# Kernel optimization log

Measured on AMD Instinct MI355X. Metric: run time of the kernel, lower is better.

## Reference

```python
import jax, jax.numpy as jnp
import numpy as np

D_MODEL = 1024
H = 16
D_K = D_MODEL // H
B = 128   # batch (intersample attention attends across this dim)
N = 256   # samples / tokens per row


def setup_inputs() -> dict:
    key = jax.random.key(0)
    ks = jax.random.split(key, 8)
    s = 1.0 / np.sqrt(D_MODEL)
    return {
        "query": jax.random.normal(ks[0], (B, N, D_MODEL), jnp.float32),
        "key":   jax.random.normal(ks[1], (B, N, D_MODEL), jnp.float32),
        "value": jax.random.normal(ks[2], (B, N, D_MODEL), jnp.float32),
        "Wq": jax.random.normal(ks[3], (D_MODEL, D_MODEL), jnp.float32) * s,
        "bq": jnp.zeros((D_MODEL,), jnp.float32),
        "Wk": jax.random.normal(ks[4], (D_MODEL, D_MODEL), jnp.float32) * s,
        "bk": jnp.zeros((D_MODEL,), jnp.float32),
        "Wv": jax.random.normal(ks[5], (D_MODEL, D_MODEL), jnp.float32) * s,
        "bv": jnp.zeros((D_MODEL,), jnp.float32),
        "Wo": jax.random.normal(ks[6], (D_MODEL, D_MODEL), jnp.float32) * s,
        "bo": jnp.zeros((D_MODEL,), jnp.float32),
    }


def _proj_heads(x, W, b):
    # torch nn.Linear: x @ W.T + b ; then view (b, n, h, d_k) -> (b, h, n, d_k)
    y = jnp.einsum('bnd,ed->bne', x, W) + b
    bsz, n, _ = y.shape
    return y.reshape(bsz, n, H, D_K).transpose(0, 2, 1, 3)


def reference(query, key, value, Wq, bq, Wk, bk, Wv, bv, Wo, bo):
    q = _proj_heads(query, Wq, bq)  # (b, h, n, d_k)
    k = _proj_heads(key,   Wk, bk)
    v = _proj_heads(value, Wv, bv)
    # intersample attention: attend ACROSS the batch dim b (per head, per sample n)
    scale = 1.0 / jnp.sqrt(jnp.asarray(D_K, q.dtype))
    scores = jnp.einsum('bhnd,chnd->hnbc', q, k) * scale  # (h, n, b, b)
    p = jax.nn.softmax(scores, axis=-1)
    out = jnp.einsum('hnbc,chnd->bhnd', p, v)             # (b, h, n, d_k)
    # merge heads: (b, h, n, d_k) -> (b, n, h*d_k)
    bsz, _, n, _ = out.shape
    out = out.transpose(0, 2, 1, 3).reshape(bsz, n, H * D_K)
    return jnp.einsum('bnd,ed->bne', out, Wo) + bo
```

## Files before the change

kernel.cpp:

```cpp
#include <hip/hip_runtime.h>
#include <hip/hip_bf16.h>
#include <stdint.h>

#define D_MODEL 1024
#define HEADS   16
#define DK      64
#define BATCH   128
#define NTOK    256
#define MROWS   (BATCH * NTOK)

typedef __attribute__((ext_vector_type(8))) short bf16x8;
typedef __attribute__((ext_vector_type(4))) float f32x4;

__device__ __forceinline__ unsigned short f2b_rne(float f) {
    union { float f; unsigned int u; } c; c.f = f;
    unsigned int u = c.u;
    unsigned int r = (u + 0x7FFFu + ((u >> 16) & 1u)) >> 16;
    return (unsigned short)r;
}

__device__ __forceinline__ void async16(const void* g, void* l) {
    __builtin_amdgcn_global_load_lds(
        (__attribute__((address_space(1))) void*)g,
        (__attribute__((address_space(3))) void*)l,
        16, 0, 0);
}

__global__ __launch_bounds__(256)
void f2b_kernel(const float* __restrict__ x, ushort* __restrict__ y, int n4) {
    int i = blockIdx.x * blockDim.x + threadIdx.x;
    int stride = gridDim.x * blockDim.x;
    for (; i < n4; i += stride) {
        float4 v = ((const float4*)x)[i];
        ushort4 o;
        o.x = f2b_rne(v.x); o.y = f2b_rne(v.y);
        o.z = f2b_rne(v.z); o.w = f2b_rne(v.w);
        ((ushort4*)y)[i] = o;
    }
}

template<int MODE>
__global__ __launch_bounds__(256)
void gemm_nt(const ushort* __restrict__ A, const ushort* __restrict__ B,
             const float* __restrict__ bias, void* __restrict__ Cout,
             int M, int N, int K, float alpha)
{
    __shared__ ushort As[128 * 32];
    __shared__ ushort Bs[128 * 32];

    const int tid  = threadIdx.x;
    const int wave = tid >> 6, lane = tid & 63;
    const int quad = lane >> 4, l15 = lane & 15;
    const int pm = blockIdx.x * 128, pn = blockIdx.y * 128;
    const int wm = (wave & 1) * 64, wn = (wave >> 1) * 64;

    f32x4 acc[4][4] = {};

    const int rg = lane >> 2;
    const int c8 = (lane & 3) * 8;
    const ushort* Abase0 = A + (size_t)(pm + wave * 32 + rg) * K + c8;
    const ushort* Abase1 = Abase0 + (size_t)16 * K;
    const ushort* Bbase0 = B + (size_t)(pn + wave * 32 + rg) * K + c8;
    const ushort* Bbase1 = Bbase0 + (size_t)16 * K;

    for (int k0 = 0; k0 < K; k0 += 32) {
        __syncthreads();
        async16(Abase0 + k0, &As[wave * 1024]);
        async16(Abase1 + k0, &As[wave * 1024 + 512]);
        async16(Bbase0 + k0, &Bs[wave * 1024]);
        async16(Bbase1 + k0, &Bs[wave * 1024 + 512]);
        __syncthreads();

        bf16x8 af[4], bfr[4];
        #pragma unroll
        for (int t = 0; t < 4; t++) {
            af[t]  = *(const bf16x8*)&As[(wm + t * 16 + l15) * 32 + quad * 8];
            bfr[t] = *(const bf16x8*)&Bs[(wn + t * 16 + l15) * 32 + quad * 8];
        }
        #pragma unroll
        for (int i = 0; i < 4; i++)
            #pragma unroll
            for (int j = 0; j < 4; j++)
                acc[i][j] = __builtin_amdgcn_mfma_f32_16x16x32_bf16(af[i], bfr[j], acc[i][j], 0, 0, 0);
    }

    if (MODE == 0) {
        ushort* out = (ushort*)Cout;
        #pragma unroll
        for (int i = 0; i < 4; i++) {
            const int mbase = pm + wm + i * 16 + quad * 4;
            #pragma unroll
            for (int j = 0; j < 4; j++) {
                const int e = pn + wn + j * 16 + l15;
                const float bv = bias[e];
                const int h = e >> 6, d = e & 63;
                #pragma unroll
                for (int r = 0; r < 4; r++) {
                    const int mm = mbase + r;
                    const int bb = mm >> 8, nn = mm & 255;
                    float val = (acc[i][j][r] + bv) * alpha;
                    out[(size_t)(((h << 8) + nn) * 128 + bb) * 64 + d] = f2b_rne(val);
                }
            }
        }
    } else {
        float* out = (float*)Cout;
        #pragma unroll
        for (int i = 0; i < 4; i++) {
            const int mbase = pm + wm + i * 16 + quad * 4;
            #pragma unroll
            for (int j = 0; j < 4; j++) {
                const int e = pn + wn + j * 16 + l15;
                const float bv = bias[e];
                #pragma unroll
                for (int r = 0; r < 4; r++) {
                    const int mm = mbase + r;
                    out[(size_t)mm * N + e] = acc[i][j][r] + bv;
                }
            }
        }
    }
}

__global__ __launch_bounds__(256)
void attn_kernel(const ushort* __restrict__ Qp, const ushort* __restrict__ Kp,
                 const ushort* __restrict__ Vp, ushort* __restrict__ Ob)
{
    __shared__ ushort sm[24576];

    const int tid  = threadIdx.x;
    const int wave = tid >> 6, lane = tid & 63;
    const int quad = lane >> 4, l15 = lane & 15;
    const int hn = blockIdx.x;
    const int h = hn >> 8, n = hn & 255;
    const size_t base = (size_t)hn * (BATCH * DK);

    {
        const uint4* Qg = (const uint4*)(Qp + base);
        const uint4* Kg = (const uint4*)(Kp + base);
        uint4* s4 = (uint4*)sm;
        #pragma unroll
        for (int i = 0; i < 4; i++) {
            int id = tid + i * 256;
            s4[id]        = Qg[id];
            s4[1024 + id] = Kg[id];
        }
        const uint4* Vg = (const uint4*)(Vp + base);
        #pragma unroll
        for (int i = 0; i < 4; i++) {
            int id = tid + i * 256;
            int c = id >> 3, d8 = (id & 7) * 8;
            uint4 vv = Vg[id];
            const ushort* vs = (const ushort*)&vv;
            #pragma unroll
            for (int j = 0; j < 8; j++)
                sm[16384 + (d8 + j) * 128 + c] = vs[j];
        }
    }
    __syncthreads();

    f32x4 accs[2][8] = {};
    #pragma unroll
    for (int kk = 0; kk < 64; kk += 32) {
        bf16x8 aq[2], bk8[8];
        #pragma unroll
        for (int mt = 0; mt < 2; mt++)
            aq[mt] = *(const bf16x8*)&sm[(wave * 32 + mt * 16 + l15) * 64 + kk + quad * 8];
        #pragma unroll
        for (int nt = 0; nt < 8; nt++)
            bk8[nt] = *(const bf16x8*)&sm[8192 + (nt * 16 + l15) * 64 + kk + quad * 8];
        #pragma unroll
        for (int mt = 0; mt < 2; mt++)
            #pragma unroll
            for (int nt = 0; nt < 8; nt++)
                accs[mt][nt] = __builtin_amdgcn_mfma_f32_16x16x32_bf16(aq[mt], bk8[nt], accs[mt][nt], 0, 0, 0);
    }

    #pragma unroll
    for (int mt = 0; mt < 2; mt++) {
        #pragma unroll
        for (int r = 0; r < 4; r++) {
            float mx = accs[mt][0][r];
            #pragma unroll
            for (int nt = 1; nt < 8; nt++) mx = fmaxf(mx, accs[mt][nt][r]);
            #pragma unroll
            for (int s = 1; s < 16; s <<= 1) mx = fmaxf(mx, __shfl_xor(mx, s, 64));
            float sum = 0.f;
            #pragma unroll
            for (int nt = 0; nt < 8; nt++) {
                float e = __expf(accs[mt][nt][r] - mx);
                accs[mt][nt][r] = e;
                sum += e;
            }
            #pragma unroll
            for (int s = 1; s < 16; s <<= 1) sum += __shfl_xor(sum, s, 64);
            float inv = 1.0f / sum;
            #pragma unroll
            for (int nt = 0; nt < 8; nt++) accs[mt][nt][r] *= inv;
        }
    }

    __syncthreads();

    #pragma unroll
    for (int mt = 0; mt < 2; mt++)
        #pragma unroll
        for (int nt = 0; nt < 8; nt++)
            #pragma unroll
            for (int r = 0; r < 4; r++)
                sm[(wave * 32 + mt * 16 + quad * 4 + r) * 128 + nt * 16 + l15] =
                    f2b_rne(accs[mt][nt][r]);
    __syncthreads();

    f32x4 acco[2][4] = {};
    #pragma unroll
    for (int kk = 0; kk < 128; kk += 32) {
        bf16x8 ap[2], bv8[4];
        #pragma unroll
        for (int mt = 0; mt < 2; mt++)
            ap[mt] = *(const bf16x8*)&sm[(wave * 32 + mt * 16 + l15) * 128 + kk + quad * 8];
        #pragma unroll
        for (int nt = 0; nt < 4; nt++)
            bv8[nt] = *(const bf16x8*)&sm[16384 + (nt * 16 + l15) * 128 + kk + quad * 8];
        #pragma unroll
        for (int mt = 0; mt < 2; mt++)
            #pragma unroll
            for (int nt = 0; nt < 4; nt++)
                acco[mt][nt] = __builtin_amdgcn_mfma_f32_16x16x32_bf16(ap[mt], bv8[nt], acco[mt][nt], 0, 0, 0);
    }

    #pragma unroll
    for (int mt = 0; mt < 2; mt++)
        #pragma unroll
        for (int nt = 0; nt < 4; nt++)
            #pragma unroll
            for (int r = 0; r < 4; r++) {
                int b = wave * 32 + mt * 16 + quad * 4 + r;
                int d = nt * 16 + l15;
                Ob[((size_t)b * NTOK + n) * D_MODEL + h * DK + d] = f2b_rne(acco[mt][nt][r]);
            }
}

extern "C" void kernel_launch(void* const* d_in, const int* in_sizes, int n_in,
                              void* d_out, int out_size, void* d_ws, size_t ws_size,
                              hipStream_t stream)
{
    const float* q  = (const float*)d_in[0];
    const float* k  = (const float*)d_in[1];
    const float* v  = (const float*)d_in[2];
    const float* Wq = (const float*)d_in[3];
    const float* bq = (const float*)d_in[4];
    const float* Wk = (const float*)d_in[5];
    const float* bk = (const float*)d_in[6];
    const float* Wv = (const float*)d_in[7];
    const float* bv = (const float*)d_in[8];
    const float* Wo = (const float*)d_in[9];
    const float* bo = (const float*)d_in[10];

    const int XE = MROWS * D_MODEL;
    const int WE = D_MODEL * D_MODEL;

    ushort* xb = (ushort*)d_ws;
    ushort* Kp = xb + (size_t)XE;
    ushort* Vp = Kp + (size_t)XE;
    ushort* Wb = Vp + (size_t)XE;
    ushort* Qp = (ushort*)d_out;

    dim3 blk(256);
    dim3 ggemm(MROWS / 128, D_MODEL / 128);

    f2b_kernel<<<dim3(512),  blk, 0, stream>>>(Wq, Wb + 0 * (size_t)WE, WE / 4);
    f2b_kernel<<<dim3(512),  blk, 0, stream>>>(Wk, Wb + 1 * (size_t)WE, WE / 4);
    f2b_kernel<<<dim3(512),  blk, 0, stream>>>(Wv, Wb + 2 * (size_t)WE, WE / 4);
    f2b_kernel<<<dim3(512),  blk, 0, stream>>>(Wo, Wb + 3 * (size_t)WE, WE / 4);

    f2b_kernel<<<dim3(4096), blk, 0, stream>>>(q, xb, XE / 4);
    gemm_nt<0><<<ggemm, blk, 0, stream>>>(xb, Wb + 0 * (size_t)WE, bq, Qp,
                                          MROWS, D_MODEL, D_MODEL, 0.125f);
    f2b_kernel<<<dim3(4096), blk, 0, stream>>>(k, xb, XE / 4);
    gemm_nt<0><<<ggemm, blk, 0, stream>>>(xb, Wb + 1 * (size_t)WE, bk, Kp,
                                          MROWS, D_MODEL, D_MODEL, 1.0f);
    f2b_kernel<<<dim3(4096), blk, 0, stream>>>(v, xb, XE / 4);
    gemm_nt<0><<<ggemm, blk, 0, stream>>>(xb, Wb + 2 * (size_t)WE, bv, Vp,
                                          MROWS, D_MODEL, D_MODEL, 1.0f);

    attn_kernel<<<dim3(HEADS * NTOK), blk, 0, stream>>>(Qp, Kp, Vp, xb);

    gemm_nt<1><<<ggemm, blk, 0, stream>>>(xb, Wb + 3 * (size_t)WE, bo, d_out,
                                          MROWS, D_MODEL, D_MODEL, 1.0f);
}
```

Baseline: 1.019 ms.

## Rewrite projection GEMM as 256x256 double-buffered, swizzled, 8-wave pipelined kernel

```diff
diff --git a/kernel.cpp b/kernel.cpp
--- a/kernel.cpp
+++ b/kernel.cpp
@@ -40,65 +40,138 @@
 }
 
 template<int MODE>
-__global__ __launch_bounds__(256)
+__global__ __launch_bounds__(512, 2)
 void gemm_nt(const ushort* __restrict__ A, const ushort* __restrict__ B,
              const float* __restrict__ bias, void* __restrict__ Cout,
              int M, int N, int K, float alpha)
 {
-    __shared__ ushort As[128 * 32];
-    __shared__ ushort Bs[128 * 32];
+    __shared__ ushort smem[65536];
 
     const int tid  = threadIdx.x;
     const int wave = tid >> 6, lane = tid & 63;
     const int quad = lane >> 4, l15 = lane & 15;
-    const int pm = blockIdx.x * 128, pn = blockIdx.y * 128;
-    const int wm = (wave & 1) * 64, wn = (wave >> 1) * 64;
-
-    f32x4 acc[4][4] = {};
-
-    const int rg = lane >> 2;
-    const int c8 = (lane & 3) * 8;
-    const ushort* Abase0 = A + (size_t)(pm + wave * 32 + rg) * K + c8;
-    const ushort* Abase1 = Abase0 + (size_t)16 * K;
-    const ushort* Bbase0 = B + (size_t)(pn + wave * 32 + rg) * K + c8;
-    const ushort* Bbase1 = Bbase0 + (size_t)16 * K;
-
-    for (int k0 = 0; k0 < K; k0 += 32) {
-        __syncthreads();
-        async16(Abase0 + k0, &As[wave * 1024]);
-        async16(Abase1 + k0, &As[wave * 1024 + 512]);
-        async16(Bbase0 + k0, &Bs[wave * 1024]);
-        async16(Bbase1 + k0, &Bs[wave * 1024 + 512]);
-        __syncthreads();
-
-        bf16x8 af[4], bfr[4];
-        #pragma unroll
-        for (int t = 0; t < 4; t++) {
-            af[t]  = *(const bf16x8*)&As[(wm + t * 16 + l15) * 32 + quad * 8];
-            bfr[t] = *(const bf16x8*)&Bs[(wn + t * 16 + l15) * 32 + quad * 8];
-        }
-        #pragma unroll
-        for (int i = 0; i < 4; i++)
-            #pragma unroll
-            for (int j = 0; j < 4; j++)
-                acc[i][j] = __builtin_amdgcn_mfma_f32_16x16x32_bf16(af[i], bfr[j], acc[i][j], 0, 0, 0);
-    }
+    const int swz  = l15 & 7;
+
+    const int o  = blockIdx.x;
+    const int s  = (o & 7) * 64 + (o >> 3);
+    const int pm = (s >> 2) * 256;
+    const int pn = (s & 3) * 256;
+
+    const int arow = (wave >> 2) * 128;
+    const int brow = (wave & 3) * 64;
+
+    const size_t laneoff = (size_t)(lane >> 3) * K
+                         + (size_t)(((lane & 7) ^ (lane >> 3)) << 3);
+    const ushort* Ab = A + (size_t)(pm + wave * 32) * K + laneoff;
+    const ushort* Bb = B + (size_t)(pn + wave * 32) * K + laneoff;
+
+    f32x4 acc[8][4] = {};
+    bf16x8 afrag[4], bfrag[4];
+
+#define STAGE(BUF, kt) do {                                                     \
+    const ushort* ag_ = Ab + (size_t)(kt) * 64;                                 \
+    const ushort* bg_ = Bb + (size_t)(kt) * 64;                                 \
+    _Pragma("unroll")                                                           \
+    for (int i_ = 0; i_ < 4; ++i_) {                                            \
+        async16(ag_ + (size_t)(i_ * 8) * K,                                     \
+                &smem[(BUF) * 32768 + wave * 2048 + i_ * 512]);                 \
+        async16(bg_ + (size_t)(i_ * 8) * K,                                     \
+                &smem[(BUF) * 32768 + 16384 + wave * 2048 + i_ * 512]);         \
+    }                                                                           \
+} while (0)
+
+#define LDB(BUF, kkidx) do {                                                    \
+    _Pragma("unroll")                                                           \
+    for (int n_ = 0; n_ < 4; ++n_)                                              \
+        bfrag[n_] = *(const bf16x8*)&smem[(BUF) * 32768 + 16384                 \
+            + (brow + n_ * 16 + l15) * 64                                       \
+            + ((((kkidx) * 4 + quad) ^ swz) << 3)];                             \
+} while (0)
+
+#define LDA(BUF, kkidx, qm) do {                                                \
+    _Pragma("unroll")                                                           \
+    for (int m_ = 0; m_ < 4; ++m_)                                              \
+        afrag[m_] = *(const bf16x8*)&smem[(BUF) * 32768                         \
+            + (arow + ((qm) * 4 + m_) * 16 + l15) * 64                          \
+            + ((((kkidx) * 4 + quad) ^ swz) << 3)];                             \
+} while (0)
+
+#define MFMA16(qm) do {                                                         \
+    __builtin_amdgcn_s_setprio(1);                                              \
+    _Pragma("unroll")                                                           \
+    for (int m_ = 0; m_ < 4; ++m_)                                              \
+        _Pragma("unroll")                                                       \
+        for (int n_ = 0; n_ < 4; ++n_)                                          \
+            acc[(qm) * 4 + m_][n_] = __builtin_amdgcn_mfma_f32_16x16x32_bf16(   \
+                afrag[m_], bfrag[n_], acc[(qm) * 4 + m_][n_], 0, 0, 0);         \
+    __builtin_amdgcn_s_setprio(0);                                              \
+} while (0)
+
+#define PHASE_STD(BUF, kkidx, qm, RB) do {                                      \
+    if (RB) LDB(BUF, kkidx);                                                    \
+    LDA(BUF, kkidx, qm);                                                        \
+    __builtin_amdgcn_s_barrier();                                               \
+    asm volatile("s_waitcnt lgkmcnt(0)" ::: "memory");                          \
+    __builtin_amdgcn_sched_barrier(0);                                          \
+    MFMA16(qm);                                                                 \
+    __builtin_amdgcn_s_barrier();                                               \
+} while (0)
+
+#define PHASE_LAST(BUF, kt, vmN) do {                                           \
+    LDA(BUF, 1, 1);                                                             \
+    asm volatile("s_waitcnt lgkmcnt(0)" ::: "memory");                          \
+    __builtin_amdgcn_sched_barrier(0);                                          \
+    __builtin_amdgcn_s_barrier();                                               \
+    if ((kt) >= 0) STAGE(BUF, kt);                                              \
+    MFMA16(1);                                                                  \
+    if ((vmN) == 8)      { asm volatile("s_waitcnt vmcnt(8)" ::: "memory"); }   \
+    else if ((vmN) == 0) { asm volatile("s_waitcnt vmcnt(0)" ::: "memory"); }   \
+    __builtin_amdgcn_sched_barrier(0);                                          \
+    __builtin_amdgcn_s_barrier();                                               \
+} while (0)
+
+    STAGE(0, 0);
+    STAGE(1, 1);
+    asm volatile("s_waitcnt vmcnt(8)" ::: "memory");
+    __builtin_amdgcn_sched_barrier(0);
+    __builtin_amdgcn_s_barrier();
+
+    #pragma unroll 1
+    for (int it = 0; it < 8; ++it) {
+        const int t2 = 2 * it + 2;
+        const int t3 = 2 * it + 3;
+        PHASE_STD(0, 0, 0, 1);
+        PHASE_STD(0, 0, 1, 0);
+        PHASE_STD(0, 1, 0, 1);
+        PHASE_LAST(0, (t2 < 16) ? t2 : -1, (t2 < 16) ? 8 : 0);
+        PHASE_STD(1, 0, 0, 1);
+        PHASE_STD(1, 0, 1, 0);
+        PHASE_STD(1, 1, 0, 1);
+        PHASE_LAST(1, (t3 < 16) ? t3 : -1, (t3 < 16) ? 8 : -1);
+    }
+
+#undef PHASE_LAST
+#undef PHASE_STD
+#undef MFMA16
+#undef LDA
+#undef LDB
+#undef STAGE
 
     if (MODE == 0) {
         ushort* out = (ushort*)Cout;
         #pragma unroll
-        for (int i = 0; i < 4; i++) {
-            const int mbase = pm + wm + i * 16 + quad * 4;
-            #pragma unroll
-            for (int j = 0; j < 4; j++) {
-                const int e = pn + wn + j * 16 + l15;
+        for (int m = 0; m < 8; ++m) {
+            const int mbase = pm + arow + m * 16 + quad * 4;
+            #pragma unroll
+            for (int n = 0; n < 4; ++n) {
+                const int e = pn + brow + n * 16 + l15;
                 const float bv = bias[e];
                 const int h = e >> 6, d = e & 63;
                 #pragma unroll
-                for (int r = 0; r < 4; r++) {
+                for (int r = 0; r < 4; ++r) {
                     const int mm = mbase + r;
                     const int bb = mm >> 8, nn = mm & 255;
-                    float val = (acc[i][j][r] + bv) * alpha;
+                    float val = (acc[m][n][r] + bv) * alpha;
                     out[(size_t)(((h << 8) + nn) * 128 + bb) * 64 + d] = f2b_rne(val);
                 }
             }
@@ -106,16 +179,16 @@
     } else {
         float* out = (float*)Cout;
         #pragma unroll
-        for (int i = 0; i < 4; i++) {
-            const int mbase = pm + wm + i * 16 + quad * 4;
-            #pragma unroll
-            for (int j = 0; j < 4; j++) {
-                const int e = pn + wn + j * 16 + l15;
+        for (int m = 0; m < 8; ++m) {
+            const int mbase = pm + arow + m * 16 + quad * 4;
+            #pragma unroll
+            for (int n = 0; n < 4; ++n) {
+                const int e = pn + brow + n * 16 + l15;
                 const float bv = bias[e];
                 #pragma unroll
-                for (int r = 0; r < 4; r++) {
+                for (int r = 0; r < 4; ++r) {
                     const int mm = mbase + r;
-                    out[(size_t)mm * N + e] = acc[i][j][r] + bv;
+                    out[(size_t)mm * N + e] = acc[m][n][r] + bv;
                 }
             }
         }
@@ -267,7 +340,8 @@
     ushort* Qp = (ushort*)d_out;
 
     dim3 blk(256);
-    dim3 ggemm(MROWS / 128, D_MODEL / 128);
+    dim3 gblk(512);
+    dim3 ggemm(512);
 
     f2b_kernel<<<dim3(512),  blk, 0, stream>>>(Wq, Wb + 0 * (size_t)WE, WE / 4);
     f2b_kernel<<<dim3(512),  blk, 0, stream>>>(Wk, Wb + 1 * (size_t)WE, WE / 4);
@@ -275,17 +349,17 @@
     f2b_kernel<<<dim3(512),  blk, 0, stream>>>(Wo, Wb + 3 * (size_t)WE, WE / 4);
 
     f2b_kernel<<<dim3(4096), blk, 0, stream>>>(q, xb, XE / 4);
-    gemm_nt<0><<<ggemm, blk, 0, stream>>>(xb, Wb + 0 * (size_t)WE, bq, Qp,
-                                          MROWS, D_MODEL, D_MODEL, 0.125f);
+    gemm_nt<0><<<ggemm, gblk, 0, stream>>>(xb, Wb + 0 * (size_t)WE, bq, Qp,
+                                           MROWS, D_MODEL, D_MODEL, 0.125f);
     f2b_kernel<<<dim3(4096), blk, 0, stream>>>(k, xb, XE / 4);
-    gemm_nt<0><<<ggemm, blk, 0, stream>>>(xb, Wb + 1 * (size_t)WE, bk, Kp,
-                                          MROWS, D_MODEL, D_MODEL, 1.0f);
+    gemm_nt<0><<<ggemm, gblk, 0, stream>>>(xb, Wb + 1 * (size_t)WE, bk, Kp,
+                                           MROWS, D_MODEL, D_MODEL, 1.0f);
     f2b_kernel<<<dim3(4096), blk, 0, stream>>>(v, xb, XE / 4);
-    gemm_nt<0><<<ggemm, blk, 0, stream>>>(xb, Wb + 2 * (size_t)WE, bv, Vp,
-                                          MROWS, D_MODEL, D_MODEL, 1.0f);
+    gemm_nt<0><<<ggemm, gblk, 0, stream>>>(xb, Wb + 2 * (size_t)WE, bv, Vp,
+                                           MROWS, D_MODEL, D_MODEL, 1.0f);
 
     attn_kernel<<<dim3(HEADS * NTOK), blk, 0, stream>>>(Qp, Kp, Vp, xb);
 
-    gemm_nt<1><<<ggemm, blk, 0, stream>>>(xb, Wb + 3 * (size_t)WE, bo, d_out,
-                                          MROWS, D_MODEL, D_MODEL, 1.0f);
-}
+    gemm_nt<1><<<ggemm, gblk, 0, stream>>>(xb, Wb + 3 * (size_t)WE, bo, d_out,
+                                           MROWS, D_MODEL, D_MODEL, 1.0f);
+}
```

Result: faster. 820.3 us (-19.5%).
